# Optimization experiments

Measured on AMD Instinct MI355X. Metric: run time of the kernel, lower is better.

## Reference

```python
import jax, jax.numpy as jnp
import numpy as np

NUM_HEADS = 32
HEAD_DIM = 64  # C = 3 * NUM_HEADS * HEAD_DIM = 6144
SCALE = NUM_HEADS ** (-0.5)


def setup_inputs() -> dict:
    key = jax.random.key(0)
    B, N, C = 4, 4096, 3 * NUM_HEADS * HEAD_DIM
    x = jax.random.normal(key, (B, N, C), dtype=jnp.float32)
    return {"x": x}


def reference(x):
    B, N, C = x.shape
    # (B, N, 3, H, d) -> (3, B, H, N, d)
    qkv = x.reshape(B, N, 3, NUM_HEADS, HEAD_DIM).transpose(2, 0, 3, 1, 4)
    q, k, v = qkv[0], qkv[1], qkv[2]
    q = q * SCALE
    # kv = k^T @ v : (B, H, d, d)
    kv = jnp.einsum('bhnd,bhne->bhde', k, v)
    kv = jax.nn.softmax(kv, axis=-1)  # dropout p=0.0 -> identity
    # attn = q @ kv^T : (B, H, N, d)
    attn = jnp.einsum('bhnd,bhed->bhne', q, kv)
    # (B, H, N, d) -> (B, N, H*d)
    out = attn.transpose(0, 2, 1, 3).reshape(B, N, NUM_HEADS * HEAD_DIM)
    return out
```

## Files before the change

### kernel.cpp

```cpp
#include <hip/hip_runtime.h>
#include <math.h>


#define NN 4096
#define CC 6144
#define QSCALE 0.17677669529663687f

#define NCHUNK 8
#define ROWS_PER_BLOCK 512

typedef __attribute__((ext_vector_type(8))) short bf16x8;
typedef __attribute__((ext_vector_type(4))) float f32x4;

static __device__ __forceinline__ unsigned short f2bf(float f) {
  unsigned u = __float_as_uint(f);
  u = (u + 0x7FFFu + ((u >> 16) & 1u)) >> 16;
  return (unsigned short)u;
}

__global__ __launch_bounds__(256) void k1_kv_accum(const float* __restrict__ x,
                                                   float* __restrict__ ws1) {
  __shared__ float lds[4096];

  const int bid = blockIdx.x;
  const int bh = bid >> 3;
  const int chunk = bid & (NCHUNK - 1);
  const int b = bh >> 5, h = bh & 31;

  const int t = threadIdx.x;
  const int lane = t & 63;
  const int w = t >> 6;
  const int ag = lane & 7;
  const int cg = lane >> 3;
  const int wbase = w * 1024;
  const int seg = (lane & 15) * 4;
  const int srow = lane >> 4;

  float acc[8][8];
#pragma unroll
  for (int i = 0; i < 8; ++i)
#pragma unroll
    for (int j = 0; j < 8; ++j) acc[i][j] = 0.f;

  const long long row0 = (long long)b * NN + (long long)chunk * ROWS_PER_BLOCK +
                         (long long)w * 128;
  const float* kbase = x + row0 * CC + 2048 + h * 64;
  const float* vbase = x + row0 * CC + 4096 + h * 64;

#define K1_ISSUE(s, bb)                                                                   \
  do {                                                                                    \
    const long long roff = (long long)((s) * 4 + srow) * CC + seg;                        \
    __builtin_amdgcn_global_load_lds(                                                     \
        (const __attribute__((address_space(1))) void*)(kbase + roff),                    \
        (__attribute__((address_space(3))) void*)&lds[wbase + (bb) * 512 + lane * 4],     \
        16, 0, 0);                                                                        \
    __builtin_amdgcn_global_load_lds(                                                     \
        (const __attribute__((address_space(1))) void*)(vbase + roff),                    \
        (__attribute__((address_space(3))) void*)&lds[wbase + (bb) * 512 + 256 + lane * 4],\
        16, 0, 0);                                                                        \
  } while (0)

#define K1_CONSUME(bb)                                                                    \
  do {                                                                                    \
    _Pragma("unroll") for (int rr = 0; rr < 4; ++rr) {                                    \
      const int kb = wbase + (bb) * 512 + rr * 64;                                        \
      const float4 k0 = *(const float4*)&lds[kb + ag * 8];                                \
      const float4 k1 = *(const float4*)&lds[kb + ag * 8 + 4];                            \
      const float4 v0 = *(const float4*)&lds[kb + 256 + cg * 8];                          \
      const float4 v1 = *(const float4*)&lds[kb + 256 + cg * 8 + 4];                      \
      const float kk[8] = {k0.x, k0.y, k0.z, k0.w, k1.x, k1.y, k1.z, k1.w};               \
      const float vv[8] = {v0.x, v0.y, v0.z, v0.w, v1.x, v1.y, v1.z, v1.w};               \
      _Pragma("unroll") for (int i = 0; i < 8; ++i)                                       \
          _Pragma("unroll") for (int j = 0; j < 8; ++j) acc[i][j] += kk[i] * vv[j];       \
    }                                                                                     \
  } while (0)

  K1_ISSUE(0, 0);
  for (int s = 0; s < 32; ++s) {
    const int cb = s & 1;
    if (s + 1 < 32) {
      K1_ISSUE(s + 1, cb ^ 1);
      asm volatile("s_waitcnt vmcnt(2)" ::: "memory");
    } else {
      asm volatile("s_waitcnt vmcnt(0)" ::: "memory");
    }
    K1_CONSUME(cb);
  }

  __syncthreads();
  float* accl = lds;
  const int cell = (ag << 3) | cg;
  if (w == 0) {
#pragma unroll
    for (int i = 0; i < 8; ++i)
#pragma unroll
      for (int j = 0; j < 8; ++j) accl[i * 512 + j * 64 + cell] = acc[i][j];
  }
  __syncthreads();
  for (int ww = 1; ww < 4; ++ww) {
    if (w == ww) {
#pragma unroll
      for (int i = 0; i < 8; ++i)
#pragma unroll
        for (int j = 0; j < 8; ++j) accl[i * 512 + j * 64 + cell] += acc[i][j];
    }
    __syncthreads();
  }

  float* dst = ws1 + (long long)bid * 4096;
#pragma unroll
  for (int u = 0; u < 4; ++u) {
    *(float4*)&dst[u * 1024 + t * 4] = *(const float4*)&accl[u * 1024 + t * 4];
  }
}

__global__ __launch_bounds__(256) void k2_softmax(const float* __restrict__ ws1,
                                                  unsigned short* __restrict__ ws2bf) {
  const int bh = blockIdx.x;
  __shared__ float Cs[64 * 65];
  __shared__ float Ss[64 * 65];
  const int t = threadIdx.x;
  const float* src = ws1 + (long long)bh * NCHUNK * 4096;
  for (int s0 = t; s0 < 1024; s0 += 256) {
    float4 sum = {0.f, 0.f, 0.f, 0.f};
#pragma unroll
    for (int c = 0; c < NCHUNK; ++c) {
      const float4 f = *(const float4*)&src[c * 4096 + s0 * 4];
      sum.x += f.x; sum.y += f.y; sum.z += f.z; sum.w += f.w;
    }
    const float se[4] = {sum.x, sum.y, sum.z, sum.w};
#pragma unroll
    for (int e = 0; e < 4; ++e) {
      const int idx = s0 * 4 + e;
      const int i = idx >> 9;
      const int j = (idx >> 6) & 7;
      const int ag = (idx >> 3) & 7;
      const int cg = idx & 7;
      Cs[(ag * 8 + i) * 65 + (cg * 8 + j)] = se[e];
    }
  }
  __syncthreads();
  if (t < 64) {
    const int a = t;
    float m = -3.0e38f;
    for (int c = 0; c < 64; ++c) m = fmaxf(m, Cs[a * 65 + c]);
    float sum = 0.f;
    for (int c = 0; c < 64; ++c) {
      const float e = expf(Cs[a * 65 + c] - m);
      Ss[a * 65 + c] = e;
      sum += e;
    }
    const float inv = QSCALE / sum;
    for (int c = 0; c < 64; ++c) Ss[a * 65 + c] *= inv;
  }
  __syncthreads();
  unsigned short* dst = ws2bf + (long long)bh * 4096;
  for (int idx = t; idx < 4096; idx += 256) {
    const int j = idx >> 6;
    const int i = idx & 63;
    dst[idx] = f2bf(Ss[j * 65 + i]);
  }
}

__global__ __launch_bounds__(256) void k3_apply(const float* __restrict__ x,
                                                const unsigned short* __restrict__ ws2bf,
                                                float* __restrict__ out) {
  const int bid = blockIdx.x;
  const int bh = bid >> 5;
  const int tile = bid & 31;
  const int b = bh >> 5, h = bh & 31;
  const int t = threadIdx.x;
  const int lane = t & 63;
  const int w = t >> 6;
  const int bn = lane & 15;
  const int g = lane >> 4;

  const unsigned short* mb = ws2bf + (long long)bh * 4096;
  bf16x8 afr[4][2];
#pragma unroll
  for (int mt = 0; mt < 4; ++mt)
#pragma unroll
    for (int kc = 0; kc < 2; ++kc)
      afr[mt][kc] = *(const bf16x8*)(mb + (mt * 16 + bn) * 64 + kc * 32 + g * 8);

  const float* qb = x + ((long long)b * NN + tile * 128) * CC + h * 64;
  bf16x8 bfr[2][2];
#pragma unroll
  for (int u = 0; u < 2; ++u) {
    const int nt = w * 2 + u;
#pragma unroll
    for (int kc = 0; kc < 2; ++kc) {
      const float* p = qb + (long long)(nt * 16 + bn) * CC + kc * 32 + g * 8;
      const float4 f0 = *(const float4*)p;
      const float4 f1 = *(const float4*)(p + 4);
      bf16x8 r;
      r[0] = (short)f2bf(f0.x); r[1] = (short)f2bf(f0.y);
      r[2] = (short)f2bf(f0.z); r[3] = (short)f2bf(f0.w);
      r[4] = (short)f2bf(f1.x); r[5] = (short)f2bf(f1.y);
      r[6] = (short)f2bf(f1.z); r[7] = (short)f2bf(f1.w);
      bfr[u][kc] = r;
    }
  }

  f32x4 acc[2][4];
#pragma unroll
  for (int u = 0; u < 2; ++u)
#pragma unroll
    for (int mt = 0; mt < 4; ++mt) acc[u][mt] = (f32x4){0.f, 0.f, 0.f, 0.f};

#pragma unroll
  for (int kc = 0; kc < 2; ++kc)
#pragma unroll
    for (int u = 0; u < 2; ++u)
#pragma unroll
      for (int mt = 0; mt < 4; ++mt)
        acc[u][mt] = __builtin_amdgcn_mfma_f32_16x16x32_bf16(afr[mt][kc], bfr[u][kc],
                                                             acc[u][mt], 0, 0, 0);

  const long long rowg = (long long)b * NN + tile * 128;
#pragma unroll
  for (int u = 0; u < 2; ++u) {
    const int nt = w * 2 + u;
    const long long r = rowg + nt * 16 + bn;
#pragma unroll
    for (int mt = 0; mt < 4; ++mt) {
      float* op = out + r * 2048 + h * 64 + mt * 16 + g * 4;
      const float4 o = {acc[u][mt][0], acc[u][mt][1], acc[u][mt][2], acc[u][mt][3]};
      *(float4*)op = o;
    }
  }
}

extern "C" void kernel_launch(void* const* d_in, const int* in_sizes, int n_in,
                              void* d_out, int out_size, void* d_ws, size_t ws_size,
                              hipStream_t stream) {
  const float* x = (const float*)d_in[0];
  float* out = (float*)d_out;
  float* ws1 = (float*)d_ws;
  unsigned short* ws2bf = (unsigned short*)(ws1 + (size_t)128 * NCHUNK * 4096);

  k1_kv_accum<<<128 * NCHUNK, 256, 0, stream>>>(x, ws1);
  k2_softmax<<<128, 256, 0, stream>>>(ws1, ws2bf);
  k3_apply<<<128 * 32, 256, 0, stream>>>(x, ws2bf, out);
}
```

Measured before the change: 148.1 us.

## Compute K^T V with split-bf16 MFMA instead of scalar FP32 FMAs

Rewrites the K^T·V accumulation kernel to use 16x16x32 bf16 MFMA instructions. Each FP32 value is split into hi and lo bf16 parts, and three MFMAs (hh, hl, lh) stand in for a full FP32 product. Global-to-LDS loads become 4-byte transposing loads into double-buffered LDS, and each wave owns output tiles, so the cross-wave LDS reduction is gone. The accumulator layout becomes row-major and the softmax kernel's index mapping is updated to match. The risks are the lower precision from the 3-term split and the narrow 4-byte load granularity.

```diff
diff --git a/kernel.cpp b/kernel.cpp
--- a/kernel.cpp
+++ b/kernel.cpp
@@ -5,9 +5,7 @@
 #define NN 4096
 #define CC 6144
 #define QSCALE 0.17677669529663687f
-
 #define NCHUNK 8
-#define ROWS_PER_BLOCK 512
 
 typedef __attribute__((ext_vector_type(8))) short bf16x8;
 typedef __attribute__((ext_vector_type(4))) float f32x4;
@@ -18,100 +16,100 @@
   return (unsigned short)u;
 }
 
-__global__ __launch_bounds__(256) void k1_kv_accum(const float* __restrict__ x,
-                                                   float* __restrict__ ws1) {
-  __shared__ float lds[4096];
+__global__ __launch_bounds__(256, 4) void k1_kv_accum(const float* __restrict__ x,
+                                                      float* __restrict__ ws1) {
+  __shared__ float lds[2][4096];
 
   const int bid = blockIdx.x;
   const int bh = bid >> 3;
   const int chunk = bid & (NCHUNK - 1);
   const int b = bh >> 5, h = bh & 31;
-
   const int t = threadIdx.x;
   const int lane = t & 63;
   const int w = t >> 6;
-  const int ag = lane & 7;
-  const int cg = lane >> 3;
-  const int wbase = w * 1024;
-  const int seg = (lane & 15) * 4;
-  const int srow = lane >> 4;
-
-  float acc[8][8];
-#pragma unroll
-  for (int i = 0; i < 8; ++i)
-#pragma unroll
-    for (int j = 0; j < 8; ++j) acc[i][j] = 0.f;
-
-  const long long row0 = (long long)b * NN + (long long)chunk * ROWS_PER_BLOCK +
-                         (long long)w * 128;
+
+  const long long row0 = (long long)b * NN + (long long)chunk * 512;
   const float* kbase = x + row0 * CC + 2048 + h * 64;
-  const float* vbase = x + row0 * CC + 4096 + h * 64;
-
-#define K1_ISSUE(s, bb)                                                                   \
+  const float* kl = kbase + (lane & 3) * CC + (lane >> 2) + w * 16;
+  const float* vl = kl + 2048;
+
+#define K1_STAGE(sb, bbv)                                                                 \
   do {                                                                                    \
-    const long long roff = (long long)((s) * 4 + srow) * CC + seg;                        \
-    __builtin_amdgcn_global_load_lds(                                                     \
-        (const __attribute__((address_space(1))) void*)(kbase + roff),                    \
-        (__attribute__((address_space(3))) void*)&lds[wbase + (bb) * 512 + lane * 4],     \
-        16, 0, 0);                                                                        \
-    __builtin_amdgcn_global_load_lds(                                                     \
-        (const __attribute__((address_space(1))) void*)(vbase + roff),                    \
-        (__attribute__((address_space(3))) void*)&lds[wbase + (bb) * 512 + 256 + lane * 4],\
-        16, 0, 0);                                                                        \
-  } while (0)
-
-#define K1_CONSUME(bb)                                                                    \
-  do {                                                                                    \
-    _Pragma("unroll") for (int rr = 0; rr < 4; ++rr) {                                    \
-      const int kb = wbase + (bb) * 512 + rr * 64;                                        \
-      const float4 k0 = *(const float4*)&lds[kb + ag * 8];                                \
-      const float4 k1 = *(const float4*)&lds[kb + ag * 8 + 4];                            \
-      const float4 v0 = *(const float4*)&lds[kb + 256 + cg * 8];                          \
-      const float4 v1 = *(const float4*)&lds[kb + 256 + cg * 8 + 4];                      \
-      const float kk[8] = {k0.x, k0.y, k0.z, k0.w, k1.x, k1.y, k1.z, k1.w};               \
-      const float vv[8] = {v0.x, v0.y, v0.z, v0.w, v1.x, v1.y, v1.z, v1.w};               \
-      _Pragma("unroll") for (int i = 0; i < 8; ++i)                                       \
-          _Pragma("unroll") for (int j = 0; j < 8; ++j) acc[i][j] += kk[i] * vv[j];       \
+    const float* kp_ = kl + (sb) * 32 * CC;                                               \
+    const float* vp_ = vl + (sb) * 32 * CC;                                               \
+    _Pragma("unroll") for (int r_ = 0; r_ < 2; ++r_)                                      \
+    _Pragma("unroll") for (int sub_ = 0; sub_ < 4; ++sub_) {                              \
+      const int ro_ = (sub_ * 8 + r_ * 4) * CC;                                           \
+      const int li_ = w * 512 + r_ * 256 + sub_ * 64;                                     \
+      __builtin_amdgcn_global_load_lds(                                                   \
+          (const __attribute__((address_space(1))) void*)(kp_ + ro_),                     \
+          (__attribute__((address_space(3))) void*)&lds[(bbv)][li_], 4, 0, 0);            \
+      __builtin_amdgcn_global_load_lds(                                                   \
+          (const __attribute__((address_space(1))) void*)(vp_ + ro_),                     \
+          (__attribute__((address_space(3))) void*)&lds[(bbv)][2048 + li_], 4, 0, 0);     \
     }                                                                                     \
   } while (0)
 
-  K1_ISSUE(0, 0);
-  for (int s = 0; s < 32; ++s) {
-    const int cb = s & 1;
-    if (s + 1 < 32) {
-      K1_ISSUE(s + 1, cb ^ 1);
-      asm volatile("s_waitcnt vmcnt(2)" ::: "memory");
-    } else {
+#define K1_FRAG(bbv, baseidx, hi8, lo8)                                                   \
+  do {                                                                                    \
+    const float4 f0_ = *(const float4*)&lds[(bbv)][(baseidx) + lane * 4];                 \
+    const float4 f1_ = *(const float4*)&lds[(bbv)][(baseidx) + 256 + lane * 4];           \
+    const float ff_[8] = {f0_.x, f0_.y, f0_.z, f0_.w, f1_.x, f1_.y, f1_.z, f1_.w};        \
+    _Pragma("unroll") for (int e_ = 0; e_ < 8; ++e_) {                                    \
+      const unsigned u_ = __float_as_uint(ff_[e_]);                                       \
+      hi8[e_] = (short)(u_ >> 16);       \
+      const float lof_ = ff_[e_] - __uint_as_float(u_ & 0xFFFF0000u);                     \
+      lo8[e_] = (short)(__float_as_uint(lof_) >> 16);                                     \
+    }                                                                                     \
+  } while (0)
+
+  f32x4 acc[2][2];
+#pragma unroll
+  for (int i2 = 0; i2 < 2; ++i2)
+#pragma unroll
+    for (int j2 = 0; j2 < 2; ++j2) acc[i2][j2] = (f32x4){0.f, 0.f, 0.f, 0.f};
+
+  const int mt0 = (w & 1) * 2;
+  const int nt0 = (w >> 1) * 2;
+
+  K1_STAGE(0, 0);
+  asm volatile("s_waitcnt vmcnt(0)" ::: "memory");
+  __syncthreads();
+
+  for (int s = 0; s < 16; ++s) {
+    const int bb = s & 1;
+    if (s + 1 < 16) K1_STAGE(s + 1, bb ^ 1);
+
+    bf16x8 ah[2], al[2], bh8[2], bl8[2];
+#pragma unroll
+    for (int i2 = 0; i2 < 2; ++i2) K1_FRAG(bb, (mt0 + i2) * 512, ah[i2], al[i2]);
+#pragma unroll
+    for (int j2 = 0; j2 < 2; ++j2) K1_FRAG(bb, 2048 + (nt0 + j2) * 512, bh8[j2], bl8[j2]);
+
+#pragma unroll
+    for (int i2 = 0; i2 < 2; ++i2)
+#pragma unroll
+      for (int j2 = 0; j2 < 2; ++j2) {
+        acc[i2][j2] = __builtin_amdgcn_mfma_f32_16x16x32_bf16(ah[i2], bh8[j2], acc[i2][j2], 0, 0, 0);
+        acc[i2][j2] = __builtin_amdgcn_mfma_f32_16x16x32_bf16(ah[i2], bl8[j2], acc[i2][j2], 0, 0, 0);
+        acc[i2][j2] = __builtin_amdgcn_mfma_f32_16x16x32_bf16(al[i2], bh8[j2], acc[i2][j2], 0, 0, 0);
+      }
+
+    if (s + 1 < 16) {
       asm volatile("s_waitcnt vmcnt(0)" ::: "memory");
-    }
-    K1_CONSUME(cb);
-  }
-
-  __syncthreads();
-  float* accl = lds;
-  const int cell = (ag << 3) | cg;
-  if (w == 0) {
-#pragma unroll
-    for (int i = 0; i < 8; ++i)
-#pragma unroll
-      for (int j = 0; j < 8; ++j) accl[i * 512 + j * 64 + cell] = acc[i][j];
-  }
-  __syncthreads();
-  for (int ww = 1; ww < 4; ++ww) {
-    if (w == ww) {
-#pragma unroll
-      for (int i = 0; i < 8; ++i)
-#pragma unroll
-        for (int j = 0; j < 8; ++j) accl[i * 512 + j * 64 + cell] += acc[i][j];
-    }
-    __syncthreads();
+      __syncthreads();
+    }
   }
 
   float* dst = ws1 + (long long)bid * 4096;
-#pragma unroll
-  for (int u = 0; u < 4; ++u) {
-    *(float4*)&dst[u * 1024 + t * 4] = *(const float4*)&accl[u * 1024 + t * 4];
-  }
+  const int g = lane >> 4, cl = lane & 15;
+#pragma unroll
+  for (int i2 = 0; i2 < 2; ++i2)
+#pragma unroll
+    for (int j2 = 0; j2 < 2; ++j2)
+#pragma unroll
+      for (int r = 0; r < 4; ++r)
+        dst[((mt0 + i2) * 16 + g * 4 + r) * 64 + (nt0 + j2) * 16 + cl] = acc[i2][j2][r];
 }
 
 __global__ __launch_bounds__(256) void k2_softmax(const float* __restrict__ ws1,
@@ -132,11 +130,7 @@
 #pragma unroll
     for (int e = 0; e < 4; ++e) {
       const int idx = s0 * 4 + e;
-      const int i = idx >> 9;
-      const int j = (idx >> 6) & 7;
-      const int ag = (idx >> 3) & 7;
-      const int cg = idx & 7;
-      Cs[(ag * 8 + i) * 65 + (cg * 8 + j)] = se[e];
+      Cs[(idx >> 6) * 65 + (idx & 63)] = se[e];
     }
   }
   __syncthreads();
```

Measured after the change: 148.9 us, median of 2. Within noise of the previous version (+0.5%).
